# Kernel tuning notes

Hardware: AMD Instinct MI355X
Metric: run time of the kernel (lower is better)

## Reference

```python
import jax, jax.numpy as jnp
import numpy as np

PATCH = 11
STRIDE = 2
WIN_SIGMA = 1.5
C1 = 0.01 ** 2
C2 = 0.03 ** 2


def gauss_win():
    # 1D gaussian (matches _fspecial_gauss_1d) outer-producted to a 2D window
    # over the p*p patch pixels (separable SSIM window), flattened to (p*p,).
    coords = jnp.arange(PATCH, dtype=jnp.float32) - PATCH // 2
    g = jnp.exp(-(coords ** 2) / (2.0 * WIN_SIGMA ** 2))
    g = g / g.sum()
    return jnp.outer(g, g).reshape(-1)


def extract_patches(im):
    # im: (B,3,H,W) -> (B, n_patches, 3, p*p); feature dim of
    # conv_general_dilated_patches is channel-major (C, p, p).
    pat = jax.lax.conv_general_dilated_patches(
        im, (PATCH, PATCH), (STRIDE, STRIDE), 'VALID')  # (B, 3*p*p, H', W')
    B = im.shape[0]
    pat = pat.reshape(B, 3, PATCH * PATCH, -1)
    return jnp.transpose(pat, (0, 3, 1, 2))


def mmd_ssim(xp, yp, win):
    # xp: (M,3,pp), yp: (N,3,pp). Returns scalar MMD = s^T K s, where
    # K is the pairwise SSIM kernel matrix and s the scale vector.
    M, N = xp.shape[0], yp.shape[0]
    s = jnp.concatenate([jnp.full((N,), 1.0 / N, jnp.float32),
                         jnp.full((M,), -1.0 / M, jnp.float32)])
    X = jnp.concatenate([xp, yp], axis=0)
    X = (X + 1.0) / 2.0
    Xw = X * win                                   # (P,3,pp)
    mus = Xw.sum(-1)                               # (P,3)
    mus_sq = mus ** 2
    sigmas = (Xw * X).sum(-1) - mus_sq             # (P,3)
    sig_sum = sigmas[:, None] + sigmas[None, :]    # (P,P,3)
    mus_sum = mus_sq[:, None] + mus_sq[None, :]
    mus_mult = mus_sq[:, None] * mus_sq[None, :]
    sigmas_xy = jnp.einsum('icp,jcp->ijc', Xw, X) - mus_mult
    cs_map = (2.0 * sigmas_xy + C2) / (sig_sum + C2)
    ssim_map = (2.0 * mus_mult + C1) / (mus_sum + C1) * cs_map
    K = ssim_map.mean(-1)                          # (P,P)
    return s @ (K @ s)


def setup_inputs() -> dict:
    key = jax.random.key(0)
    kx, ky = jax.random.split(key)
    x = jax.random.normal(kx, (2, 3, 80, 80), dtype=jnp.float32)
    y = jax.random.normal(ky, (2, 3, 80, 80), dtype=jnp.float32)
    return {"x": x, "y": y}


def reference(x, y):
    win = gauss_win()
    xp = extract_patches(x)  # (B, P, 3, pp)
    yp = extract_patches(y)
    losses = jax.vmap(lambda a, b: mmd_ssim(a, b, win))(xp, yp)  # (B,)
    return losses.mean()  # batch_reduction='mean'
```

## Files before the change

kernel.cpp:

```cpp
#include <hip/hip_runtime.h>
#include <math.h>

#define PATCH   11
#define PP      121
#define NPX     35
#define NPATCH  1225
#define P2      2450
#define NC      3
#define NB      2
#define NROW    2560
#define NKC     16
#define RT      128
#define CT      64
#define NSTRIP  (NROW/RT)
#define NCT     (NROW/CT)
#define C1f     1.0e-4f
#define C2f     9.0e-4f

typedef _Float16 f16;
typedef __attribute__((ext_vector_type(8)))  _Float16 f16x8;
typedef __attribute__((ext_vector_type(16))) float    f32x16;

__global__ __launch_bounds__(256) void extract_kernel(
        const float* __restrict__ x, const float* __restrict__ y,
        f16* __restrict__ Zh, f16* __restrict__ Zl,
        float2* __restrict__ msig, double* __restrict__ acc) {
    int t = threadIdx.x, lane = t & 63, w = t >> 6;
    int i  = blockIdx.x * 16 + w * 4 + (lane >> 4);
    int kc = lane & 15;
    int c = blockIdx.y, b = blockIdx.z;
    if (t == 0 && blockIdx.x == 0 && c == 0 && b == 0) acc[0] = 0.0;

    int bc = b * NC + c;
    bool valid = (i < P2);

    float g1[PATCH]; float gs = 0.f;
#pragma unroll
    for (int k = 0; k < PATCH; k++) {
        float d = (float)(k - PATCH / 2);
        g1[k] = expf(-(d * d) / 4.5f);
        gs += g1[k];
    }
    float inv2 = 1.0f / (gs * gs);

    const float* base = x;
    if (valid) {
        const float* img = (i < NPATCH) ? x : y;
        int ip = (i < NPATCH) ? i : i - NPATCH;
        int py = ip / NPX, px = ip - py * NPX;
        base = img + ((size_t)bc * 80 + py * 2) * 80 + px * 2;
    }

    float mu = 0.f, e2 = 0.f;
    f16x8 hv = {}, lv = {};
#pragma unroll
    for (int q = 0; q < 8; q++) {
        int p = kc * 8 + q;
        float z = 0.f;
        if (valid && p < PP) {
            int r = p / PATCH, s = p - (p / PATCH) * PATCH;
            float wg = g1[r] * g1[s] * inv2;
            float X = (base[r * 80 + s] + 1.0f) * 0.5f;
            mu = fmaf(wg, X, mu);
            e2 = fmaf(wg * X, X, e2);
            z = sqrtf(wg) * X;
        }
        f16 h = (f16)z;
        hv[q] = h;
        lv[q] = (f16)(z - (float)h);
    }
    size_t off = (((size_t)bc * NKC + kc) * NROW + i) * 8;
    *(f16x8*)(Zh + off) = hv;
    *(f16x8*)(Zl + off) = lv;

#pragma unroll
    for (int m = 1; m < 16; m <<= 1) {
        mu += __shfl_xor(mu, m);
        e2 += __shfl_xor(e2, m);
    }
    if (kc == 0) {
        float m2 = mu * mu;
        msig[(size_t)bc * NROW + i] = make_float2(m2, e2 - m2);
    }
}

__global__ __launch_bounds__(256) void pair_kernel(
        const f16* __restrict__ Zh, const f16* __restrict__ Zl,
        const float2* __restrict__ msig, double* __restrict__ acc) {
    int tj = blockIdx.x, si = blockIdx.y, b = blockIdx.z;
    if (tj < 2 * si) return;

    int t = threadIdx.x, lane = t & 63, w = t >> 6;
    int lr = lane & 31, hi = lane >> 5;
    int R0 = si * RT + w * 32;

    double local = 0.0;

    for (int c = 0; c < NC; c++) {
        int bc = b * NC + c;
        const f16* zh = Zh + (size_t)bc * NKC * NROW * 8;
        const f16* zl = Zl + (size_t)bc * NKC * NROW * 8;
        const float2* ms = msig + (size_t)bc * NROW;

        f16x8 Ah[8];
#pragma unroll
        for (int ks = 0; ks < 8; ks++)
            Ah[ks] = *(const f16x8*)(zh + ((size_t)(ks * 2 + hi) * NROW + R0 + lr) * 8);

#pragma unroll
        for (int cb = 0; cb < 2; cb++) {
            int C0 = tj * CT + cb * 32;
            f32x16 a = {};
#pragma unroll
            for (int ks = 0; ks < 8; ks++) {
                size_t ko = (size_t)(ks * 2 + hi) * NROW;
                f16x8 bh = *(const f16x8*)(zh + (ko + C0 + lr) * 8);
                f16x8 bl = *(const f16x8*)(zl + (ko + C0 + lr) * 8);
                f16x8 al = *(const f16x8*)(zl + (ko + R0 + lr) * 8);
                a = __builtin_amdgcn_mfma_f32_32x32x16_f16(Ah[ks], bh, a, 0, 0, 0);
                a = __builtin_amdgcn_mfma_f32_32x32x16_f16(Ah[ks], bl, a, 0, 0, 0);
                a = __builtin_amdgcn_mfma_f32_32x32x16_f16(al,     bh, a, 0, 0, 0);
            }

            int gj = C0 + lr;
            float2 mj = ms[gj];
            bool yj = gj < NPATCH;
#pragma unroll
            for (int reg = 0; reg < 16; reg++) {
                int gi = R0 + (reg & 3) + 8 * (reg >> 2) + 4 * hi;
                float2 mi = ms[gi];
                float mm  = mi.x * mj.x;
                float sxy = a[reg] - mm;
                float num = (2.f * mm + C1f) * (2.f * sxy + C2f);
                float den = (mi.x + mj.x + C1f) * (mi.y + mj.y + C2f);
                float kv  = num * __builtin_amdgcn_rcpf(den);
                float wgt = (gj > gi) ? 2.f : ((gj == gi) ? 1.f : 0.f);
                if (gi >= P2 || gj >= P2) wgt = 0.f;
                float sgn = ((gi < NPATCH) == yj) ? 1.f : -1.f;
                local += (double)(wgt * sgn * kv);
            }
        }
    }

#pragma unroll
    for (int off = 32; off > 0; off >>= 1)
        local += __shfl_down(local, off);
    __shared__ double red[4];
    if (lane == 0) red[w] = local;
    __syncthreads();
    if (t == 0)
        atomicAdd(acc, red[0] + red[1] + red[2] + red[3]);
}

__global__ void finalize_kernel(const double* __restrict__ acc,
                                float* __restrict__ out) {
    if (threadIdx.x == 0 && blockIdx.x == 0)
        out[0] = (float)(acc[0] * (1.0 / (2.0 * 3.0 * (double)NPATCH * (double)NPATCH)));
}

extern "C" void kernel_launch(void* const* d_in, const int* in_sizes, int n_in,
                              void* d_out, int out_size, void* d_ws, size_t ws_size,
                              hipStream_t stream) {
    const float* x = (const float*)d_in[0];
    const float* y = (const float*)d_in[1];
    float* out = (float*)d_out;

    double* acc = (double*)d_ws;
    f16* Zh = (f16*)((char*)d_ws + 16);
    size_t zcnt = (size_t)NB * NC * NKC * NROW * 8;
    f16* Zl = Zh + zcnt;
    float2* msig = (float2*)(Zl + zcnt);

    dim3 g1(NROW / 16, NC, NB);
    extract_kernel<<<g1, 256, 0, stream>>>(x, y, Zh, Zl, msig, acc);

    dim3 g2(NCT, NSTRIP, NB);
    pair_kernel<<<g2, 256, 0, stream>>>(Zh, Zl, msig, acc);

    finalize_kernel<<<1, 64, 0, stream>>>(acc, out);
}
```

Measured before the change: 115.8 us.

## Stage B tiles in LDS, compact triangular grid, skip lower tiles

Stages the column tile of Zh/Zl into shared memory with global_load_lds, so the four waves share one copy instead of each reading it from global memory. The A low-part fragments are preloaded into registers. The grid is compacted to only the upper-triangular tile pairs, found by a small index-decoding loop, which removes the blocks that used to exit immediately. 32-column sub-tiles lying entirely below the diagonal are skipped, and launch bounds now request 4 blocks per CU. The cost is extra register pressure, added barriers, and 32KB of LDS per block.

```diff
diff --git a/kernel.cpp b/kernel.cpp
--- a/kernel.cpp
+++ b/kernel.cpp
@@ -14,12 +14,19 @@
 #define CT      64
 #define NSTRIP  (NROW/RT)
 #define NCT     (NROW/CT)
+#define WPAIR   420
 #define C1f     1.0e-4f
 #define C2f     9.0e-4f
 
 typedef _Float16 f16;
 typedef __attribute__((ext_vector_type(8)))  _Float16 f16x8;
 typedef __attribute__((ext_vector_type(16))) float    f32x16;
+
+__device__ __forceinline__ void gload16(const void* g, void* l) {
+    __builtin_amdgcn_global_load_lds((const __attribute__((address_space(1))) void*)(g),
+                                     (__attribute__((address_space(3))) void*)(l),
+                                     16, 0, 0);
+}
 
 __global__ __launch_bounds__(256) void extract_kernel(
         const float* __restrict__ x, const float* __restrict__ y,
@@ -84,13 +91,18 @@
     }
 }
 
-__global__ __launch_bounds__(256) void pair_kernel(
+__global__ __launch_bounds__(256, 4) void pair_kernel(
         const f16* __restrict__ Zh, const f16* __restrict__ Zl,
         const float2* __restrict__ msig, double* __restrict__ acc) {
-    int tj = blockIdx.x, si = blockIdx.y, b = blockIdx.z;
-    if (tj < 2 * si) return;
+    __shared__ __align__(16) f16 Bsh[2][CT * 128];
 
     int t = threadIdx.x, lane = t & 63, w = t >> 6;
+    int b = blockIdx.y;
+
+    int l = blockIdx.x, si = 0;
+    while (l >= NCT - 2 * si) { l -= NCT - 2 * si; si++; }
+    int tj = 2 * si + l;
+
     int lr = lane & 31, hi = lane >> 5;
     int R0 = si * RT + w * 32;
 
@@ -102,24 +114,39 @@
         const f16* zl = Zl + (size_t)bc * NKC * NROW * 8;
         const float2* ms = msig + (size_t)bc * NROW;
 
-        f16x8 Ah[8];
-#pragma unroll
-        for (int ks = 0; ks < 8; ks++)
-            Ah[ks] = *(const f16x8*)(zh + ((size_t)(ks * 2 + hi) * NROW + R0 + lr) * 8);
+        f16x8 Ah[8], Al[8];
+#pragma unroll
+        for (int ks = 0; ks < 8; ks++) {
+            size_t ro = ((size_t)(ks * 2 + hi) * NROW + R0 + lr) * 8;
+            Ah[ks] = *(const f16x8*)(zh + ro);
+            Al[ks] = *(const f16x8*)(zl + ro);
+        }
+
+        __syncthreads();
+#pragma unroll
+        for (int q = 0; q < 4; q++) {
+            int u = q * 256 + t;
+            int kc = u >> 6, col = u & 63;
+            size_t so = ((size_t)kc * NROW + tj * CT + col) * 8;
+            gload16(zh + so, &Bsh[0][(size_t)u * 8]);
+            gload16(zl + so, &Bsh[1][(size_t)u * 8]);
+        }
+        __syncthreads();
 
 #pragma unroll
         for (int cb = 0; cb < 2; cb++) {
             int C0 = tj * CT + cb * 32;
+            if (C0 + 31 < R0) continue;
+
             f32x16 a = {};
 #pragma unroll
             for (int ks = 0; ks < 8; ks++) {
-                size_t ko = (size_t)(ks * 2 + hi) * NROW;
-                f16x8 bh = *(const f16x8*)(zh + (ko + C0 + lr) * 8);
-                f16x8 bl = *(const f16x8*)(zl + (ko + C0 + lr) * 8);
-                f16x8 al = *(const f16x8*)(zl + (ko + R0 + lr) * 8);
+                int kc = ks * 2 + hi;
+                f16x8 bh = *(const f16x8*)&Bsh[0][(kc * 64 + cb * 32 + lr) * 8];
+                f16x8 bl = *(const f16x8*)&Bsh[1][(kc * 64 + cb * 32 + lr) * 8];
                 a = __builtin_amdgcn_mfma_f32_32x32x16_f16(Ah[ks], bh, a, 0, 0, 0);
                 a = __builtin_amdgcn_mfma_f32_32x32x16_f16(Ah[ks], bl, a, 0, 0, 0);
-                a = __builtin_amdgcn_mfma_f32_32x32x16_f16(al,     bh, a, 0, 0, 0);
+                a = __builtin_amdgcn_mfma_f32_32x32x16_f16(Al[ks], bh, a, 0, 0, 0);
             }
 
             int gj = C0 + lr;
@@ -174,7 +201,7 @@
     dim3 g1(NROW / 16, NC, NB);
     extract_kernel<<<g1, 256, 0, stream>>>(x, y, Zh, Zl, msig, acc);
 
-    dim3 g2(NCT, NSTRIP, NB);
+    dim3 g2(WPAIR, NB);
     pair_kernel<<<g2, 256, 0, stream>>>(Zh, Zl, msig, acc);
 
     finalize_kernel<<<1, 64, 0, stream>>>(acc, out);
```

Result: slower. 137.2 us (+18.5%).
